# Kernel optimization log

Measured on AMD Instinct MI355X. Metric: run time of the kernel, lower is better.

## Reference

```python
import jax, jax.numpy as jnp
import numpy as np

N = 50000      # nodes
E = 800000     # edges (before self loops)
IN = 128       # in_channels
HID = 128      # 2*out_channels
OUT = 64       # out_channels
NEG_SLOPE = 0.2


def _gat_conv(x, src, dst, W, a_src, a_dst, b, n_nodes):
    """Single-head PyG GATConv (concat=True, heads=1, self-loops already added)."""
    h = x @ W                                   # [N, F]
    alpha_s = h @ a_src                         # [N]
    alpha_d = h @ a_dst                         # [N]
    e = alpha_s[src] + alpha_d[dst]             # [E'] logits per edge j->i
    e = jnp.where(e > 0, e, NEG_SLOPE * e)      # LeakyReLU(0.2)
    # segment softmax over destination node
    m = jax.ops.segment_max(e, dst, num_segments=n_nodes)   # [N]
    w = jnp.exp(e - m[dst])                                   # [E']
    denom = jax.ops.segment_sum(w, dst, num_segments=n_nodes) # [N]
    alpha = w / denom[dst]                                     # [E']
    out = jax.ops.segment_sum(alpha[:, None] * h[src], dst, num_segments=n_nodes)
    return out + b


def _with_self_loops(edge_index, n_nodes):
    loop = jnp.arange(n_nodes, dtype=edge_index.dtype)
    src = jnp.concatenate([edge_index[0], loop])
    dst = jnp.concatenate([edge_index[1], loop])
    return src, dst


def setup_inputs() -> dict:
    key = jax.random.key(0)
    ks = jax.random.split(key, 10)
    s = 0.1
    return {
        "x": jax.random.normal(ks[0], (N, IN), jnp.float32),
        "edge_index": jax.random.randint(ks[1], (2, E), 0, N, jnp.int32),
        "W1": jax.random.normal(ks[2], (IN, HID), jnp.float32) * s,
        "a1_src": jax.random.normal(ks[3], (HID,), jnp.float32) * s,
        "a1_dst": jax.random.normal(ks[4], (HID,), jnp.float32) * s,
        "b1": jnp.zeros((HID,), jnp.float32),
        "W2": jax.random.normal(ks[5], (HID, OUT), jnp.float32) * s,
        "a2_src": jax.random.normal(ks[6], (OUT,), jnp.float32) * s,
        "a2_dst": jax.random.normal(ks[7], (OUT,), jnp.float32) * s,
        "b2": jnp.zeros((OUT,), jnp.float32),
    }


def reference(x, edge_index, W1, a1_src, a1_dst, b1, W2, a2_src, a2_dst, b2):
    src, dst = _with_self_loops(edge_index, N)
    h = _gat_conv(x, src, dst, W1, a1_src, a1_dst, b1, N)
    h = jax.nn.relu(h)
    return _gat_conv(h, src, dst, W2, a2_src, a2_dst, b2, N)
```

## Files before the change

kernel.cpp:

```cpp
#include <hip/hip_runtime.h>
#include <hip/hip_bf16.h>


#define BCAP 4096

typedef __attribute__((ext_vector_type(8))) short bf16x8;
typedef __attribute__((ext_vector_type(4))) float f32x4;

__device__ __forceinline__ unsigned short bf16bits(float f){
  __hip_bfloat16 b = __float2bfloat16(f);
  return *(unsigned short*)&b;
}
__device__ __forceinline__ float bf16lo(unsigned int v){ return __uint_as_float(v << 16); }
__device__ __forceinline__ float bf16hi(unsigned int v){ return __uint_as_float(v & 0xFFFF0000u); }
__device__ __forceinline__ float leaky_exp(float e){
  e = (e > 0.f) ? e : 0.2f*e;
  return __expf(e);
}

struct G4 { uint4 h0, h1, h2, h3; float w0, w1, w2, w3; };

template<int F>
__device__ __forceinline__ G4 gather4(int sv, float wv, int base,
    const unsigned short* __restrict__ Hin, int fl)
{
  G4 g;
  int s0 = __shfl(sv, base),   s1 = __shfl(sv, base+1);
  int s2 = __shfl(sv, base+2), s3 = __shfl(sv, base+3);
  g.w0 = __shfl(wv, base);   g.w1 = __shfl(wv, base+1);
  g.w2 = __shfl(wv, base+2); g.w3 = __shfl(wv, base+3);
  g.h0 = *(const uint4*)&Hin[(size_t)s0*F + fl*8];
  g.h1 = *(const uint4*)&Hin[(size_t)s1*F + fl*8];
  g.h2 = *(const uint4*)&Hin[(size_t)s2*F + fl*8];
  g.h3 = *(const uint4*)&Hin[(size_t)s3*F + fl*8];
  return g;
}

__device__ __forceinline__ void fma4(const G4& g, float* acc, float& dn)
{
  dn += (g.w0 + g.w1) + (g.w2 + g.w3);
  acc[0]+=g.w0*bf16lo(g.h0.x)+g.w1*bf16lo(g.h1.x)+g.w2*bf16lo(g.h2.x)+g.w3*bf16lo(g.h3.x);
  acc[1]+=g.w0*bf16hi(g.h0.x)+g.w1*bf16hi(g.h1.x)+g.w2*bf16hi(g.h2.x)+g.w3*bf16hi(g.h3.x);
  acc[2]+=g.w0*bf16lo(g.h0.y)+g.w1*bf16lo(g.h1.y)+g.w2*bf16lo(g.h2.y)+g.w3*bf16lo(g.h3.y);
  acc[3]+=g.w0*bf16hi(g.h0.y)+g.w1*bf16hi(g.h1.y)+g.w2*bf16hi(g.h2.y)+g.w3*bf16hi(g.h3.y);
  acc[4]+=g.w0*bf16lo(g.h0.z)+g.w1*bf16lo(g.h1.z)+g.w2*bf16lo(g.h2.z)+g.w3*bf16lo(g.h3.z);
  acc[5]+=g.w0*bf16hi(g.h0.z)+g.w1*bf16hi(g.h1.z)+g.w2*bf16hi(g.h2.z)+g.w3*bf16hi(g.h3.z);
  acc[6]+=g.w0*bf16lo(g.h0.w)+g.w1*bf16lo(g.h1.w)+g.w2*bf16lo(g.h2.w)+g.w3*bf16lo(g.h3.w);
  acc[7]+=g.w0*bf16hi(g.h0.w)+g.w1*bf16hi(g.h1.w)+g.w2*bf16hi(g.h2.w)+g.w3*bf16hi(g.h3.w);
}

__global__ __launch_bounds__(256) void prep_all(
    const float* __restrict__ W1, const float* __restrict__ W2,
    const float* __restrict__ a2s, const float* __restrict__ a2d,
    unsigned short* __restrict__ W1t, unsigned short* __restrict__ W2t,
    float* __restrict__ vas, float* __restrict__ vad,
    int* __restrict__ bucketCount)
{
  int b = blockIdx.x, t = threadIdx.x;
  if (b < 48){
    int idx = b*256 + t;
    if (idx < 8192){
      int n = idx >> 6, k2 = idx & 63;
      float a = W1[(size_t)(2*k2)*128 + n];
      float c = W1[(size_t)(2*k2+1)*128 + n];
      ushort2 o; o.x = bf16bits(a); o.y = bf16bits(c);
      *(ushort2*)&W1t[(size_t)n*128 + 2*k2] = o;
    } else {
      int r = idx - 8192;
      int n = r >> 6, k2 = r & 63;
      float a = W2[(size_t)(2*k2)*64 + n];
      float c = W2[(size_t)(2*k2+1)*64 + n];
      ushort2 o; o.x = bf16bits(a); o.y = bf16bits(c);
      *(ushort2*)&W2t[(size_t)n*128 + 2*k2] = o;
    }
  } else if (b == 48){
    int k = t & 127;
    const float* av = (t < 128) ? a2s : a2d;
    float* ov = (t < 128) ? vas : vad;
    float s = 0.f;
    for (int n=0; n<64; n++) s += W2[(size_t)k*64 + n] * av[n];
    ov[k] = s;
  } else {
    bucketCount[t] = 0; bucketCount[t+256] = 0;
  }
}

template<int NC, bool FUSE>
__device__ __forceinline__ void gemm_body(
    const float* __restrict__ Af, const unsigned short* __restrict__ Ah,
    const unsigned short* __restrict__ Wt,
    const float* __restrict__ avs, const float* __restrict__ avd,
    unsigned short* __restrict__ H, float* __restrict__ as_, float* __restrict__ ad_,
    int M, int rowBase, unsigned short* As, unsigned short* Ws)
{
  const int K = 128;
  int t = threadIdx.x;
  if (Af){
    #pragma unroll
    for (int i=0;i<8;i++){
      int idx = t + i*256; int r = idx>>5, k4 = idx&31;
      int grow = rowBase + r;
      float4 v = (grow<M) ? *(const float4*)&Af[(size_t)grow*K + k4*4]
                          : make_float4(0.f,0.f,0.f,0.f);
      ushort4 o; o.x=bf16bits(v.x); o.y=bf16bits(v.y); o.z=bf16bits(v.z); o.w=bf16bits(v.w);
      *(ushort4*)&As[r*136 + k4*4] = o;
    }
  } else {
    #pragma unroll
    for (int i=0;i<4;i++){
      int idx = t + i*256; int r = idx>>4, k8 = idx&15;
      int grow = rowBase + r;
      uint4 v = (grow<M) ? *(const uint4*)&Ah[(size_t)grow*K + k8*8]
                         : make_uint4(0u,0u,0u,0u);
      *(uint4*)&As[r*136 + k8*8] = v;
    }
  }
  int wave = t>>6, lane = t&63, ln = lane&15, q = lane>>4;
  f32x4 acc[NC/16];
  #pragma unroll
  for (int nt=0; nt<NC/16; nt++) acc[nt] = (f32x4){0.f,0.f,0.f,0.f};

  #pragma unroll
  for (int ch=0; ch<NC/64; ++ch){
    __syncthreads();
    #pragma unroll
    for (int i=0;i<4;i++){
      int idx = t + i*256; int n = idx>>4, k8 = idx&15;
      *(uint4*)&Ws[n*136 + k8*8] = *(const uint4*)&Wt[(size_t)(ch*64+n)*K + k8*8];
    }
    __syncthreads();
    #pragma unroll
    for (int kk=0;kk<4;kk++){
      bf16x8 a = *(const bf16x8*)&As[(wave*16+ln)*136 + kk*32 + q*8];
      #pragma unroll
      for (int nt=0; nt<4; nt++){
        bf16x8 b = *(const bf16x8*)&Ws[(nt*16+ln)*136 + kk*32 + q*8];
        acc[ch*4+nt] = __builtin_amdgcn_mfma_f32_16x16x32_bf16(a, b, acc[ch*4+nt], 0, 0, 0);
      }
    }
  }
  float asl[NC/16], adl[NC/16];
  if (FUSE){
    #pragma unroll
    for (int nt=0; nt<NC/16; nt++){ asl[nt]=avs[nt*16+ln]; adl[nt]=avd[nt*16+ln]; }
  }
  #pragma unroll
  for (int i=0;i<4;i++){
    int grow = rowBase + wave*16 + q*4 + i;
    if (grow < M){
      float ps=0.f, pd=0.f;
      #pragma unroll
      for (int nt=0; nt<NC/16; nt++){
        float v = acc[nt][i];
        H[(size_t)grow*NC + nt*16 + ln] = bf16bits(v);
        if (FUSE){ ps += v*asl[nt]; pd += v*adl[nt]; }
      }
      if (FUSE){
        #pragma unroll
        for (int d=1; d<16; d<<=1){ ps += __shfl_xor(ps,d); pd += __shfl_xor(pd,d); }
        if (ln==0){ as_[grow] = ps; ad_[grow] = pd; }
      }
    }
  }
}

__global__ __launch_bounds__(256) void scatter_or_gemm(
    const int* __restrict__ src, const int* __restrict__ dst,
    int* __restrict__ bucketCount, unsigned int* __restrict__ gbuf, int E, int SB,
    const float* __restrict__ x, const unsigned short* __restrict__ W1t,
    const float* __restrict__ a1s, const float* __restrict__ a1d,
    unsigned short* __restrict__ h1, float* __restrict__ as1, float* __restrict__ ad1,
    int M)
{
  __shared__ unsigned short smem[64*136 + 64*136];
  int t = threadIdx.x;
  if ((int)blockIdx.x >= SB){
    gemm_body<128, true>(x, nullptr, W1t, a1s, a1d, h1, as1, ad1, M,
                         (blockIdx.x - SB)*64, smem, smem + 64*136);
    return;
  }
  int* hist = (int*)smem;
  int* base = hist + 512;
  int e0 = blockIdx.x * 4096;
  hist[t] = 0; hist[t+256] = 0;
  __syncthreads();
  int sv[16], dv[16];
  #pragma unroll
  for (int k=0;k<16;k++){
    int i = e0 + t + k*256;
    if (i < E){ sv[k]=src[i]; dv[k]=dst[i]; atomicAdd(&hist[dv[k]>>7], 1); }
    else { sv[k] = -1; dv[k] = 0; }
  }
  __syncthreads();
  int h0 = hist[t], h1c = hist[t+256];
  if (h0 > 0)  base[t]     = atomicAdd(&bucketCount[t],     h0);
  if (h1c > 0) base[t+256] = atomicAdd(&bucketCount[t+256], h1c);
  __syncthreads();
  hist[t] = 0; hist[t+256] = 0;
  __syncthreads();
  #pragma unroll
  for (int k=0;k<16;k++){
    if (sv[k] >= 0){
      int b = dv[k] >> 7;
      int r = base[b] + atomicAdd(&hist[b], 1);
      if (r < BCAP)
        gbuf[(size_t)b*BCAP + r] = ((unsigned)(dv[k] & 127) << 16) | (unsigned)sv[k];
    }
  }
}

__global__ __launch_bounds__(512) void fine_sort(
    const unsigned int* __restrict__ gbuf, const int* __restrict__ bucketCount,
    int* __restrict__ offs, int* __restrict__ srcS,
    const float* __restrict__ as1, const float* __restrict__ ad1,
    float* __restrict__ wS1, unsigned short* __restrict__ dstS,
    int N, int E, int B)
{
  __shared__ int sh[512];
  __shared__ int h[128];
  __shared__ int pre[128];
  __shared__ int rank[128];
  int b = blockIdx.x, t = threadIdx.x;
  {
    int nd_t = 0;
    if (t < B){ int lo=t*128; nd_t = (N-lo<128)?(N-lo):128; }
    sh[t] = (t < B ? bucketCount[t] : 0) + nd_t;
    __syncthreads();
    for (int d=1; d<512; d<<=1){
      int x = (t >= d) ? sh[t-d] : 0;
      __syncthreads();
      sh[t] += x;
      __syncthreads();
    }
  }
  int cnt = bucketCount[b]; if (cnt > BCAP) cnt = BCAP;
  int lo = b*128;
  int nd = (N - lo < 128) ? (N - lo) : 128;
  int base = sh[b] - (cnt + nd);
  if (b == 0 && t == 0) offs[N] = E + N;
  if (t < 128){ h[t] = 0; rank[t] = 0; }
  __syncthreads();
  for (int i = t; i < cnt; i += 512)
    atomicAdd(&h[(gbuf[(size_t)b*BCAP + i] >> 16) & 127], 1);
  __syncthreads();
  if (t < 128) pre[t] = (t < nd) ? (h[t] + 1) : 0;
  __syncthreads();
  for (int d=1; d<128; d<<=1){
    int x = (t >= d && t < 128) ? pre[t-d] : 0;
    __syncthreads();
    if (t < 128) pre[t] += x;
    __syncthreads();
  }
  int seg = (t < nd) ? (h[t] + 1) : 0;
  int ex  = (t < 128) ? (pre[t] - seg) : 0;
  if (t < nd){
    int v = lo + t;
    offs[v] = base + ex;
    srcS[base + ex] = v;
    wS1[base + ex]  = leaky_exp(as1[v] + ad1[v]);
    dstS[base + ex] = (unsigned short)v;
  }
  __syncthreads();
  if (t < 128) pre[t] = ex;
  __syncthreads();
  for (int i = t; i < cnt; i += 512){
    unsigned e = gbuf[(size_t)b*BCAP + i];
    int dl = (e >> 16) & 127;
    int s  = e & 0xFFFF;
    int r  = atomicAdd(&rank[dl], 1);
    int pos = base + pre[dl] + 1 + r;
    srcS[pos] = s;
    wS1[pos]  = leaky_exp(as1[s] + ad1[lo + dl]);
    dstS[pos] = (unsigned short)(lo + dl);
  }
}

__global__ __launch_bounds__(256) void edge_agg128(
    const int* __restrict__ offs, const int* __restrict__ srcS,
    const float* __restrict__ wS,
    const unsigned short* __restrict__ Hin, const float* __restrict__ bias,
    unsigned short* __restrict__ outp,
    const float* __restrict__ vas, const float* __restrict__ vad,
    float* __restrict__ as2, float* __restrict__ ad2, int n)
{
  int wid  = (blockIdx.x * 256 + threadIdx.x) >> 6;
  int lane = threadIdx.x & 63;
  int qw = lane >> 4, ql = lane & 15;
  int v = wid*4 + qw;
  bool alive = (v < n);
  int beg = 0, end = 0;
  if (alive){ beg = offs[v]; end = offs[v+1]; }
  float acc[8] = {}; float dn = 0.f;
  int l0 = qw << 4;
  for (int base = beg; base < end; base += 8){
    int rem = end - base;
    int sv = 0; float wv = 0.f;
    if (ql < 8 && ql < rem){ sv = srcS[base + ql]; wv = wS[base + ql]; }
    G4 ga = gather4<128>(sv, wv, l0+0, Hin, ql);
    G4 gb = gather4<128>(sv, wv, l0+4, Hin, ql);
    fma4(ga, acc, dn);
    fma4(gb, acc, dn);
  }
  if (alive){
    float inv = 1.0f / dn;
    float ps = 0.f, pd = 0.f;
    unsigned short o[8];
    #pragma unroll
    for (int k=0;k<8;k++){
      float u = fmaxf(acc[k]*inv + bias[ql*8+k], 0.f);
      o[k] = bf16bits(u);
      ps += u * vas[ql*8+k];
      pd += u * vad[ql*8+k];
    }
    *(uint4*)&outp[(size_t)v*128 + ql*8] = *(uint4*)o;
    #pragma unroll
    for (int d2=1; d2<16; d2<<=1){ ps += __shfl_xor(ps,d2); pd += __shfl_xor(pd,d2); }
    if (ql == 0){ as2[v] = ps; ad2[v] = pd; }
  }
}

__global__ __launch_bounds__(256) void gemm2_or_wprep(
    const unsigned short* __restrict__ A, const unsigned short* __restrict__ Wt,
    unsigned short* __restrict__ H, int M, int G2B,
    const int* __restrict__ srcS, const unsigned short* __restrict__ dstS,
    const float* __restrict__ as2, const float* __restrict__ ad2,
    float* __restrict__ wS2, int T)
{
  __shared__ unsigned short smem[64*136 + 64*136];
  if ((int)blockIdx.x < G2B){
    gemm_body<64, false>(nullptr, A, Wt, nullptr, nullptr, H, nullptr, nullptr,
                         M, blockIdx.x*64, smem, smem + 64*136);
    return;
  }
  int i0 = (blockIdx.x - G2B)*256 + threadIdx.x;
  int stride = (gridDim.x - G2B)*256;
  for (int e = i0; e < T; e += stride){
    int s = srcS[e];
    int d = dstS[e];
    wS2[e] = leaky_exp(as2[s] + ad2[d]);
  }
}

__global__ __launch_bounds__(256) void edge_agg64(
    const int* __restrict__ offs, const int* __restrict__ srcS,
    const float* __restrict__ wS,
    const unsigned short* __restrict__ Hin, const float* __restrict__ bias,
    float* __restrict__ outp, int n)
{
  int wid  = (blockIdx.x * 256 + threadIdx.x) >> 6;
  int lane = threadIdx.x & 63;
  int ew = lane >> 3, el = lane & 7;
  int v = wid*8 + ew;
  bool alive = (v < n);
  int beg = 0, end = 0;
  if (alive){ beg = offs[v]; end = offs[v+1]; }
  float acc[8] = {}; float dn = 0.f;
  int l0 = ew << 3;
  for (int base = beg; base < end; base += 8){
    int rem = end - base;
    int sv = 0; float wv = 0.f;
    if (el < rem){ sv = srcS[base + el]; wv = wS[base + el]; }
    G4 ga = gather4<64>(sv, wv, l0+0, Hin, el);
    G4 gb = gather4<64>(sv, wv, l0+4, Hin, el);
    fma4(ga, acc, dn);
    fma4(gb, acc, dn);
  }
  if (alive){
    float inv = 1.0f / dn;
    float4 o0, o1;
    o0.x = acc[0]*inv + bias[el*8+0]; o0.y = acc[1]*inv + bias[el*8+1];
    o0.z = acc[2]*inv + bias[el*8+2]; o0.w = acc[3]*inv + bias[el*8+3];
    o1.x = acc[4]*inv + bias[el*8+4]; o1.y = acc[5]*inv + bias[el*8+5];
    o1.z = acc[6]*inv + bias[el*8+6]; o1.w = acc[7]*inv + bias[el*8+7];
    *(float4*)&outp[(size_t)v*64 + el*8]     = o0;
    *(float4*)&outp[(size_t)v*64 + el*8 + 4] = o1;
  }
}

extern "C" void kernel_launch(void* const* d_in, const int* in_sizes, int n_in,
                              void* d_out, int out_size, void* d_ws, size_t ws_size,
                              hipStream_t stream) {
  const int IN = 128, HID = 128, OUT = 64;
  const int N = in_sizes[0] / IN;
  const int E = in_sizes[1] / 2;
  const int B = (N + 127) / 128;
  const int SB = (E + 4095) / 4096;
  const int T = E + N;

  const float* x    = (const float*)d_in[0];
  const int*   ei   = (const int*)d_in[1];
  const float* W1   = (const float*)d_in[2];
  const float* a1s  = (const float*)d_in[3];
  const float* a1d  = (const float*)d_in[4];
  const float* b1   = (const float*)d_in[5];
  const float* W2   = (const float*)d_in[6];
  const float* a2s  = (const float*)d_in[7];
  const float* a2d  = (const float*)d_in[8];
  const float* b2   = (const float*)d_in[9];
  float* out = (float*)d_out;

  char* w = (char*)d_ws;
  unsigned short* W1t = (unsigned short*)w; w += (size_t)HID*IN*2;
  unsigned short* W2t = (unsigned short*)w; w += (size_t)OUT*HID*2;
  unsigned short* h1    = (unsigned short*)w; w += (size_t)N*128*2;
  unsigned short* hrelu = (unsigned short*)w; w += (size_t)N*128*2;
  unsigned short* h2 = h1;
  float* as1   = (float*)w; w += (size_t)N*4;
  float* ad1   = (float*)w; w += (size_t)N*4;
  float* as2   = (float*)w; w += (size_t)N*4;
  float* ad2   = (float*)w; w += (size_t)N*4;
  float* vas   = (float*)w; w += 128*4;
  float* vad   = (float*)w; w += 128*4;
  int* offs    = (int*)w;   w += (size_t)(N+1)*4;
  int* bucketCount = (int*)w; w += 512*4;
  int* srcS    = (int*)w;   w += (size_t)T*4;
  float* wS1   = (float*)w; w += (size_t)T*4;
  float* wS2   = (float*)w; w += (size_t)T*4;
  unsigned short* dstS = (unsigned short*)w; w += ((size_t)T*2 + 3) & ~(size_t)3;
  unsigned int* gbuf = (unsigned int*)w; w += (size_t)B*BCAP*4;

  const int* esrc = ei;
  const int* edst = ei + E;

  hipLaunchKernelGGL(prep_all, dim3(50), dim3(256), 0, stream,
                     W1, W2, a2s, a2d, W1t, W2t, vas, vad, bucketCount);
  hipLaunchKernelGGL(scatter_or_gemm, dim3(SB + (N+63)/64), dim3(256), 0, stream,
                     esrc, edst, bucketCount, gbuf, E, SB,
                     x, W1t, a1s, a1d, h1, as1, ad1, N);
  hipLaunchKernelGGL(fine_sort, dim3(B), dim3(512), 0, stream,
                     gbuf, bucketCount, offs, srcS, as1, ad1, wS1, dstS, N, E, B);
  int wv128 = (N + 3) / 4;
  hipLaunchKernelGGL(edge_agg128, dim3((wv128 + 3) / 4), dim3(256), 0, stream,
                     offs, srcS, wS1, h1, b1, hrelu, vas, vad, as2, ad2, N);
  const int G2B = (N + 63) / 64;
  hipLaunchKernelGGL(gemm2_or_wprep, dim3(G2B + 512), dim3(256), 0, stream,
                     hrelu, W2t, h2, N, G2B, srcS, dstS, as2, ad2, wS2, T);
  int wv64 = (N + 7) / 8;
  hipLaunchKernelGGL(edge_agg64, dim3((wv64 + 3) / 4), dim3(256), 0, stream,
                     offs, srcS, wS2, h2, b2, out, N);
}
```

Measured before the change: 185.9 us.

## Split edge aggregation across feature slices with software-pipelined gathers

```diff
diff --git a/kernel.cpp b/kernel.cpp
--- a/kernel.cpp
+++ b/kernel.cpp
@@ -18,43 +18,12 @@
   return __expf(e);
 }
 
-struct G4 { uint4 h0, h1, h2, h3; float w0, w1, w2, w3; };
-
-template<int F>
-__device__ __forceinline__ G4 gather4(int sv, float wv, int base,
-    const unsigned short* __restrict__ Hin, int fl)
-{
-  G4 g;
-  int s0 = __shfl(sv, base),   s1 = __shfl(sv, base+1);
-  int s2 = __shfl(sv, base+2), s3 = __shfl(sv, base+3);
-  g.w0 = __shfl(wv, base);   g.w1 = __shfl(wv, base+1);
-  g.w2 = __shfl(wv, base+2); g.w3 = __shfl(wv, base+3);
-  g.h0 = *(const uint4*)&Hin[(size_t)s0*F + fl*8];
-  g.h1 = *(const uint4*)&Hin[(size_t)s1*F + fl*8];
-  g.h2 = *(const uint4*)&Hin[(size_t)s2*F + fl*8];
-  g.h3 = *(const uint4*)&Hin[(size_t)s3*F + fl*8];
-  return g;
-}
-
-__device__ __forceinline__ void fma4(const G4& g, float* acc, float& dn)
-{
-  dn += (g.w0 + g.w1) + (g.w2 + g.w3);
-  acc[0]+=g.w0*bf16lo(g.h0.x)+g.w1*bf16lo(g.h1.x)+g.w2*bf16lo(g.h2.x)+g.w3*bf16lo(g.h3.x);
-  acc[1]+=g.w0*bf16hi(g.h0.x)+g.w1*bf16hi(g.h1.x)+g.w2*bf16hi(g.h2.x)+g.w3*bf16hi(g.h3.x);
-  acc[2]+=g.w0*bf16lo(g.h0.y)+g.w1*bf16lo(g.h1.y)+g.w2*bf16lo(g.h2.y)+g.w3*bf16lo(g.h3.y);
-  acc[3]+=g.w0*bf16hi(g.h0.y)+g.w1*bf16hi(g.h1.y)+g.w2*bf16hi(g.h2.y)+g.w3*bf16hi(g.h3.y);
-  acc[4]+=g.w0*bf16lo(g.h0.z)+g.w1*bf16lo(g.h1.z)+g.w2*bf16lo(g.h2.z)+g.w3*bf16lo(g.h3.z);
-  acc[5]+=g.w0*bf16hi(g.h0.z)+g.w1*bf16hi(g.h1.z)+g.w2*bf16hi(g.h2.z)+g.w3*bf16hi(g.h3.z);
-  acc[6]+=g.w0*bf16lo(g.h0.w)+g.w1*bf16lo(g.h1.w)+g.w2*bf16lo(g.h2.w)+g.w3*bf16lo(g.h3.w);
-  acc[7]+=g.w0*bf16hi(g.h0.w)+g.w1*bf16hi(g.h1.w)+g.w2*bf16hi(g.h2.w)+g.w3*bf16hi(g.h3.w);
-}
-
 __global__ __launch_bounds__(256) void prep_all(
     const float* __restrict__ W1, const float* __restrict__ W2,
     const float* __restrict__ a2s, const float* __restrict__ a2d,
     unsigned short* __restrict__ W1t, unsigned short* __restrict__ W2t,
     float* __restrict__ vas, float* __restrict__ vad,
-    int* __restrict__ bucketCount)
+    int* __restrict__ bucketCount, float* __restrict__ as2z, int NZ)
 {
   int b = blockIdx.x, t = threadIdx.x;
   if (b < 48){
@@ -80,8 +49,12 @@
     float s = 0.f;
     for (int n=0; n<64; n++) s += W2[(size_t)k*64 + n] * av[n];
     ov[k] = s;
+  } else if (b == 49){
+    bucketCount[t] = 0; bucketCount[t+256] = 0;
   } else {
-    bucketCount[t] = 0; bucketCount[t+256] = 0;
+    int idx = (b - 50)*256 + t;
+    if (idx < NZ)
+      *(float4*)&as2z[idx*4] = make_float4(0.f,0.f,0.f,0.f);
   }
 }
 
@@ -283,39 +256,62 @@
     const float* __restrict__ vas, const float* __restrict__ vad,
     float* __restrict__ as2, float* __restrict__ ad2, int n)
 {
-  int wid  = (blockIdx.x * 256 + threadIdx.x) >> 6;
+  int slice = blockIdx.x & 3;
+  int v = (blockIdx.x >> 2) * 16 + (threadIdx.x >> 4);
   int lane = threadIdx.x & 63;
-  int qw = lane >> 4, ql = lane & 15;
-  int v = wid*4 + qw;
+  int ql = lane & 15;
+  int er = ql >> 2;
+  int fq = ql & 3;
+  int l0 = lane & 48;
+  int fo = slice*32 + fq*8;
   bool alive = (v < n);
   int beg = 0, end = 0;
   if (alive){ beg = offs[v]; end = offs[v+1]; }
   float acc[8] = {}; float dn = 0.f;
-  int l0 = qw << 4;
-  for (int base = beg; base < end; base += 8){
-    int rem = end - base;
-    int sv = 0; float wv = 0.f;
-    if (ql < 8 && ql < rem){ sv = srcS[base + ql]; wv = wS[base + ql]; }
-    G4 ga = gather4<128>(sv, wv, l0+0, Hin, ql);
-    G4 gb = gather4<128>(sv, wv, l0+4, Hin, ql);
-    fma4(ga, acc, dn);
-    fma4(gb, acc, dn);
-  }
+  int svA = 0, svB = 0; float wvA = 0.f, wvB = 0.f;
+  if (ql < 4){
+    if (beg + ql < end)     { svA = srcS[beg+ql];   wvA = wS[beg+ql]; }
+    if (beg + 4 + ql < end) { svB = srcS[beg+4+ql]; wvB = wS[beg+4+ql]; }
+  }
+  int   s = __shfl(svA, l0 + er);
+  float w = __shfl(wvA, l0 + er);
+  uint4 h = *(const uint4*)&Hin[(size_t)s*128 + fo];
+  for (int base = beg + 4; base < end; base += 4){
+    int svC = 0; float wvC = 0.f;
+    if (ql < 4 && base + 4 + ql < end){ svC = srcS[base+4+ql]; wvC = wS[base+4+ql]; }
+    int   s2 = __shfl(svB, l0 + er);
+    float w2 = __shfl(wvB, l0 + er);
+    uint4 h2 = *(const uint4*)&Hin[(size_t)s2*128 + fo];
+    dn += w;
+    acc[0]+=w*bf16lo(h.x); acc[1]+=w*bf16hi(h.x);
+    acc[2]+=w*bf16lo(h.y); acc[3]+=w*bf16hi(h.y);
+    acc[4]+=w*bf16lo(h.z); acc[5]+=w*bf16hi(h.z);
+    acc[6]+=w*bf16lo(h.w); acc[7]+=w*bf16hi(h.w);
+    svB = svC; wvB = wvC; w = w2; h = h2;
+  }
+  dn += w;
+  acc[0]+=w*bf16lo(h.x); acc[1]+=w*bf16hi(h.x);
+  acc[2]+=w*bf16lo(h.y); acc[3]+=w*bf16hi(h.y);
+  acc[4]+=w*bf16lo(h.z); acc[5]+=w*bf16hi(h.z);
+  acc[6]+=w*bf16lo(h.w); acc[7]+=w*bf16hi(h.w);
+  dn += __shfl_xor(dn, 4); dn += __shfl_xor(dn, 8);
+  #pragma unroll
+  for (int k=0;k<8;k++){ acc[k]+=__shfl_xor(acc[k],4); acc[k]+=__shfl_xor(acc[k],8); }
   if (alive){
     float inv = 1.0f / dn;
     float ps = 0.f, pd = 0.f;
     unsigned short o[8];
     #pragma unroll
     for (int k=0;k<8;k++){
-      float u = fmaxf(acc[k]*inv + bias[ql*8+k], 0.f);
+      float u = fmaxf(acc[k]*inv + bias[fo+k], 0.f);
       o[k] = bf16bits(u);
-      ps += u * vas[ql*8+k];
-      pd += u * vad[ql*8+k];
-    }
-    *(uint4*)&outp[(size_t)v*128 + ql*8] = *(uint4*)o;
-    #pragma unroll
-    for (int d2=1; d2<16; d2<<=1){ ps += __shfl_xor(ps,d2); pd += __shfl_xor(pd,d2); }
-    if (ql == 0){ as2[v] = ps; ad2[v] = pd; }
+      ps += u * vas[fo+k];
+      pd += u * vad[fo+k];
+    }
+    if (er == 0) *(uint4*)&outp[(size_t)v*128 + fo] = *(uint4*)o;
+    ps += __shfl_xor(ps,1); ps += __shfl_xor(ps,2);
+    pd += __shfl_xor(pd,1); pd += __shfl_xor(pd,2);
+    if (ql == 0){ atomicAdd(&as2[v], ps); atomicAdd(&ad2[v], pd); }
   }
 }
 
@@ -347,33 +343,56 @@
     const unsigned short* __restrict__ Hin, const float* __restrict__ bias,
     float* __restrict__ outp, int n)
 {
-  int wid  = (blockIdx.x * 256 + threadIdx.x) >> 6;
+  int slice = blockIdx.x & 3;
+  int v = (blockIdx.x >> 2) * 32 + (threadIdx.x >> 3);
   int lane = threadIdx.x & 63;
-  int ew = lane >> 3, el = lane & 7;
-  int v = wid*8 + ew;
+  int el = lane & 7;
+  int er = el >> 1;
+  int fh = el & 1;
+  int l0 = lane & 56;
+  int fo = slice*16 + fh*8;
   bool alive = (v < n);
   int beg = 0, end = 0;
   if (alive){ beg = offs[v]; end = offs[v+1]; }
   float acc[8] = {}; float dn = 0.f;
-  int l0 = ew << 3;
-  for (int base = beg; base < end; base += 8){
-    int rem = end - base;
-    int sv = 0; float wv = 0.f;
-    if (el < rem){ sv = srcS[base + el]; wv = wS[base + el]; }
-    G4 ga = gather4<64>(sv, wv, l0+0, Hin, el);
-    G4 gb = gather4<64>(sv, wv, l0+4, Hin, el);
-    fma4(ga, acc, dn);
-    fma4(gb, acc, dn);
-  }
-  if (alive){
+  int svA = 0, svB = 0; float wvA = 0.f, wvB = 0.f;
+  if (el < 4){
+    if (beg + el < end)     { svA = srcS[beg+el];   wvA = wS[beg+el]; }
+    if (beg + 4 + el < end) { svB = srcS[beg+4+el]; wvB = wS[beg+4+el]; }
+  }
+  int   s = __shfl(svA, l0 + er);
+  float w = __shfl(wvA, l0 + er);
+  uint4 h = *(const uint4*)&Hin[(size_t)s*64 + fo];
+  for (int base = beg + 4; base < end; base += 4){
+    int svC = 0; float wvC = 0.f;
+    if (el < 4 && base + 4 + el < end){ svC = srcS[base+4+el]; wvC = wS[base+4+el]; }
+    int   s2 = __shfl(svB, l0 + er);
+    float w2 = __shfl(wvB, l0 + er);
+    uint4 h2 = *(const uint4*)&Hin[(size_t)s2*64 + fo];
+    dn += w;
+    acc[0]+=w*bf16lo(h.x); acc[1]+=w*bf16hi(h.x);
+    acc[2]+=w*bf16lo(h.y); acc[3]+=w*bf16hi(h.y);
+    acc[4]+=w*bf16lo(h.z); acc[5]+=w*bf16hi(h.z);
+    acc[6]+=w*bf16lo(h.w); acc[7]+=w*bf16hi(h.w);
+    svB = svC; wvB = wvC; w = w2; h = h2;
+  }
+  dn += w;
+  acc[0]+=w*bf16lo(h.x); acc[1]+=w*bf16hi(h.x);
+  acc[2]+=w*bf16lo(h.y); acc[3]+=w*bf16hi(h.y);
+  acc[4]+=w*bf16lo(h.z); acc[5]+=w*bf16hi(h.z);
+  acc[6]+=w*bf16lo(h.w); acc[7]+=w*bf16hi(h.w);
+  dn += __shfl_xor(dn, 2); dn += __shfl_xor(dn, 4);
+  #pragma unroll
+  for (int k=0;k<8;k++){ acc[k]+=__shfl_xor(acc[k],2); acc[k]+=__shfl_xor(acc[k],4); }
+  if (alive && er == 0){
     float inv = 1.0f / dn;
     float4 o0, o1;
-    o0.x = acc[0]*inv + bias[el*8+0]; o0.y = acc[1]*inv + bias[el*8+1];
-    o0.z = acc[2]*inv + bias[el*8+2]; o0.w = acc[3]*inv + bias[el*8+3];
-    o1.x = acc[4]*inv + bias[el*8+4]; o1.y = acc[5]*inv + bias[el*8+5];
-    o1.z = acc[6]*inv + bias[el*8+6]; o1.w = acc[7]*inv + bias[el*8+7];
-    *(float4*)&outp[(size_t)v*64 + el*8]     = o0;
-    *(float4*)&outp[(size_t)v*64 + el*8 + 4] = o1;
+    o0.x = acc[0]*inv + bias[fo+0]; o0.y = acc[1]*inv + bias[fo+1];
+    o0.z = acc[2]*inv + bias[fo+2]; o0.w = acc[3]*inv + bias[fo+3];
+    o1.x = acc[4]*inv + bias[fo+4]; o1.y = acc[5]*inv + bias[fo+5];
+    o1.z = acc[6]*inv + bias[fo+6]; o1.w = acc[7]*inv + bias[fo+7];
+    *(float4*)&outp[(size_t)v*64 + fo]     = o0;
+    *(float4*)&outp[(size_t)v*64 + fo + 4] = o1;
   }
 }
 
@@ -422,20 +441,20 @@
   const int* esrc = ei;
   const int* edst = ei + E;
 
-  hipLaunchKernelGGL(prep_all, dim3(50), dim3(256), 0, stream,
-                     W1, W2, a2s, a2d, W1t, W2t, vas, vad, bucketCount);
+  const int NZ = (2*N) / 4;
+  const int ZB = (NZ + 255) / 256;
+  hipLaunchKernelGGL(prep_all, dim3(50 + ZB), dim3(256), 0, stream,
+                     W1, W2, a2s, a2d, W1t, W2t, vas, vad, bucketCount, as2, NZ);
   hipLaunchKernelGGL(scatter_or_gemm, dim3(SB + (N+63)/64), dim3(256), 0, stream,
                      esrc, edst, bucketCount, gbuf, E, SB,
                      x, W1t, a1s, a1d, h1, as1, ad1, N);
   hipLaunchKernelGGL(fine_sort, dim3(B), dim3(512), 0, stream,
                      gbuf, bucketCount, offs, srcS, as1, ad1, wS1, dstS, N, E, B);
-  int wv128 = (N + 3) / 4;
-  hipLaunchKernelGGL(edge_agg128, dim3((wv128 + 3) / 4), dim3(256), 0, stream,
+  hipLaunchKernelGGL(edge_agg128, dim3(((N+15)/16)*4), dim3(256), 0, stream,
                      offs, srcS, wS1, h1, b1, hrelu, vas, vad, as2, ad2, N);
   const int G2B = (N + 63) / 64;
   hipLaunchKernelGGL(gemm2_or_wprep, dim3(G2B + 512), dim3(256), 0, stream,
                      hrelu, W2t, h2, N, G2B, srcS, dstS, as2, ad2, wS2, T);
-  int wv64 = (N + 7) / 8;
-  hipLaunchKernelGGL(edge_agg64, dim3((wv64 + 3) / 4), dim3(256), 0, stream,
+  hipLaunchKernelGGL(edge_agg64, dim3(((N+31)/32)*4), dim3(256), 0, stream,
                      offs, srcS, wS2, h2, b2, out, N);
 }
```

New measurement: 224.5 us. 1.21x slower.
